# Kernel optimization log

Hardware: AMD Instinct MI355X
Metric: run time of the kernel (lower is better)

Reference implementation:

```python
import jax, jax.numpy as jnp
import numpy as np

N = 40000          # nodes
E = 640000         # edges (avg degree 16)
MUL = 32           # multiplicity per irrep
SILU_GAIN = 1.6791 # e3nn normalize2mom constant for silu
SQ3 = float(np.sqrt(3.0)); SQ2 = float(np.sqrt(2.0))
C_S = float(np.sin(np.pi / 8)); C_X = float(np.cos(np.pi / 8))
INV_SQRT_NN = 1.0 / 4.0  # 1/sqrt(num_neighbors=16)


def _fctp_scalar_attr(xs, xv, W0, W1, na):
    # FullyConnectedTensorProduct(irreps, '1x0e', irreps): per-l linear scaled by
    # the scalar attr, with e3nn fan-in normalization 1/sqrt(mul_in).
    f0 = 1.0 / np.sqrt(W0.shape[0]); f1 = 1.0 / np.sqrt(W1.shape[0])
    ss = (xs @ W0) * f0 * na                                   # [N, w]
    sv = jnp.einsum('nui,uw->nwi', xv, W1) * f1 * na[..., None]  # [N, w, 3]
    return ss, sv


def _forward(node_input, node_attr, edge_index, edge_attr, edge_scalars,
             W_sc0, W_sc1, W_l10, W_l11, Wfc0, Wfc1, W_l20, W_l21):
    na = node_attr[:, :1]                               # [N,1] scalar 0e attr
    xs = node_input[:, :MUL]                            # [N,32]  0e
    xv = node_input[:, MUL:].reshape(-1, MUL, 3)        # [N,32,3] 1o

    # self-connection and first linear (both FCTP with scalar node attr)
    s_s, s_v = _fctp_scalar_attr(xs, xv, W_sc0, W_sc1, na)
    l_s, l_v = _fctp_scalar_attr(xs, xv, W_l10, W_l11, na)

    # radial MLP -> per-edge TP weights (weight_numel = 5*32 = 160)
    h = jax.nn.silu(edge_scalars @ Wfc0 / 4.0) * SILU_GAIN   # /sqrt(16)
    w = (h @ Wfc1) / 8.0                                     # /sqrt(64), [E,160]
    w0, w1, w2, w3, w4 = [w[:, k * MUL:(k + 1) * MUL] for k in range(5)]

    src, dst = edge_index[0], edge_index[1]
    xs_e = l_s[src]                                     # gather [E,32]
    xv_e = l_v[src]                                     # gather [E,32,3]
    ea0 = edge_attr[:, 0:1]                             # [E,1]  0e
    eav = edge_attr[:, 1:4]                             # [E,3]  1o

    # 'uvu' CG tensor product paths (mid irreps sorted: 64x0e + 96x1o)
    mid0 = w0 * xs_e * ea0                                             # 0e x 0e -> 0e
    mid1 = w3 * jnp.einsum('eui,ei->eu', xv_e, eav) / SQ3              # 1o x 1o -> 0e
    mid2 = (w1 * xs_e)[..., None] * eav[:, None, :]                    # 0e x 1o -> 1o
    mid3 = w2[..., None] * xv_e * ea0[..., None]                       # 1o x 0e -> 1o
    mid4 = w4[..., None] * jnp.cross(xv_e, eav[:, None, :]) / SQ2      # 1o x 1o -> 1o

    mid_s = jnp.concatenate([mid0, mid1], axis=1)                      # [E,64]
    mid_v = jnp.concatenate([mid2, mid3, mid4], axis=1)                # [E,96,3]

    # scatter-reduce to destination nodes
    node_s = jax.ops.segment_sum(mid_s, dst, num_segments=N) * INV_SQRT_NN
    node_v = jax.ops.segment_sum(mid_v, dst, num_segments=N) * INV_SQRT_NN

    # lin2: FCTP(mid, 1x0e, out)
    x2_s = (node_s @ W_l20) / np.sqrt(64.0) * na
    x2_v = jnp.einsum('nui,uw->nwi', node_v, W_l21) / np.sqrt(96.0) * na[..., None]

    # sc output mask is all ones here -> c_x = cos(pi/8) everywhere
    out_s = C_S * s_s + C_X * x2_s
    out_v = C_S * s_v + C_X * x2_v
    return jnp.concatenate([out_s, out_v.reshape(-1, MUL * 3)], axis=1)  # [N,128]


def setup_inputs() -> dict:
    key = jax.random.key(0)
    ks = jax.random.split(key, 13)
    return {
        'node_input': jax.random.normal(ks[0], (N, 128), jnp.float32),
        'node_attr': jax.random.normal(ks[1], (N, 1), jnp.float32),
        'edge_index': jax.random.randint(ks[2], (2, E), 0, N),
        'edge_attr': jax.random.normal(ks[3], (E, 4), jnp.float32),
        'edge_scalars': jax.random.normal(ks[4], (E, 16), jnp.float32),
        'W_sc0': jax.random.normal(ks[5], (32, 32), jnp.float32),
        'W_sc1': jax.random.normal(ks[6], (32, 32), jnp.float32),
        'W_l10': jax.random.normal(ks[7], (32, 32), jnp.float32),
        'W_l11': jax.random.normal(ks[8], (32, 32), jnp.float32),
        'Wfc0': jax.random.normal(ks[9], (16, 64), jnp.float32),
        'Wfc1': jax.random.normal(ks[10], (64, 160), jnp.float32),
        'W_l20': jax.random.normal(ks[11], (64, 32), jnp.float32),
        'W_l21': jax.random.normal(ks[12], (96, 32), jnp.float32),
    }


def reference(node_input, node_attr, edge_index, edge_attr, edge_scalars,
              W_sc0, W_sc1, W_l10, W_l11, Wfc0, Wfc1, W_l20, W_l21):
    return _forward(node_input, node_attr, edge_index, edge_attr, edge_scalars,
                    W_sc0, W_sc1, W_l10, W_l11, Wfc0, Wfc1, W_l20, W_l21)
```

## Files before the change

### kernel.cpp

```cpp
#include <hip/hip_runtime.h>
#include <math.h>

static constexpr float F0        = 0.17677669529663687f;
static constexpr float SILU_GAIN = 1.6791f;
static constexpr float INV_SQ3   = 0.5773502691896258f;
static constexpr float INV_SQ2   = 0.7071067811865475f;
static constexpr float C_S       = 0.3826834323650898f;
static constexpr float C_X       = 0.9238795325112867f;
static constexpr float INV_SQRT_NN = 0.25f;
static constexpr float INV8      = 0.125f;
static constexpr float INV_SQ96  = 0.10206207261596575f;

#define WAVE_SYNC() do { asm volatile("" ::: "memory"); \
                         __builtin_amdgcn_wave_barrier(); \
                         asm volatile("" ::: "memory"); } while (0)

__global__ __launch_bounds__(256) void k_node(
    const float* __restrict__ node_input, const float* __restrict__ node_attr,
    const float* __restrict__ Wsc0, const float* __restrict__ Wsc1,
    const float* __restrict__ Wl10, const float* __restrict__ Wl11,
    float* __restrict__ out, float* __restrict__ l_sv, int N)
{
    __shared__ float sW[4][32][32];
    __shared__ __align__(16) float sX[4][128];
    int tid = threadIdx.x;
    float4* sWv = (float4*)&sW[0][0][0];
    for (int i = tid; i < 256; i += 256) {
        sWv[i]       = ((const float4*)Wsc0)[i];
        sWv[256+i]   = ((const float4*)Wsc1)[i];
        sWv[512+i]   = ((const float4*)Wl10)[i];
        sWv[768+i]   = ((const float4*)Wl11)[i];
    }
    __syncthreads();
    int wave = tid >> 6, lane = tid & 63;
    int ngroups = (N + 3) >> 2;

    for (int grp = blockIdx.x; grp < ngroups; grp += gridDim.x) {
        int node = grp * 4 + wave;
        if (node >= N) continue;

        float2 v = *(const float2*)&node_input[(size_t)node*128 + lane*2];
        sX[wave][lane*2]   = v.x;
        sX[wave][lane*2+1] = v.y;
        float na = node_attr[node];
        WAVE_SYNC();

        const float* X = sX[wave];
        float g = F0 * na;
        #pragma unroll
        for (int p = 0; p < 2; p++) {
            int o = lane + p*64;
            float vs = 0.f, vl = 0.f;
            if (o < 32) {
                #pragma unroll
                for (int u = 0; u < 32; u++) {
                    float x = X[u];
                    vs = fmaf(x, sW[0][u][o], vs);
                    vl = fmaf(x, sW[2][u][o], vl);
                }
            } else {
                int f = o - 32; int w = f / 3; int i3 = f - 3*w;
                #pragma unroll
                for (int u = 0; u < 32; u++) {
                    float x = X[32 + 3*u + i3];
                    vs = fmaf(x, sW[1][u][w], vs);
                    vl = fmaf(x, sW[3][u][w], vl);
                }
            }
            out [(size_t)node*128 + o] = C_S * g * vs;
            l_sv[(size_t)node*128 + o] = g * vl;
        }
        WAVE_SYNC();
    }
}

__global__ void k_hist(const int* __restrict__ ei, int* __restrict__ deg, int E) {
    int e = blockIdx.x*256 + threadIdx.x;
    if (e < E) atomicAdd(&deg[ei[E + e]], 1);
}

__global__ void k_scan_part(const int* __restrict__ deg, int* __restrict__ offs,
                            int* __restrict__ part, int n) {
    __shared__ int tmp[1024];
    int t = threadIdx.x, i = blockIdx.x*1024 + t;
    int v = (i < n) ? deg[i] : 0;
    tmp[t] = v; __syncthreads();
    for (int d = 1; d < 1024; d <<= 1) {
        int x = (t >= d) ? tmp[t-d] : 0;
        __syncthreads();
        tmp[t] += x;
        __syncthreads();
    }
    if (i < n) offs[i] = tmp[t] - v;
    if (t == 1023) part[blockIdx.x] = tmp[1023];
}

__global__ void k_scan_top(int* part, int* offs, int nb, int n) {
    if (threadIdx.x == 0 && blockIdx.x == 0) {
        int run = 0;
        for (int b = 0; b < nb; b++) { int v = part[b]; part[b] = run; run += v; }
        offs[n] = run;
    }
}

__global__ void k_scan_add(int* offs, const int* part, int n) {
    int i = blockIdx.x*256 + threadIdx.x;
    if (i < n) offs[i] += part[i >> 10];
}

__global__ void k_fill(const int* __restrict__ ei, const int* __restrict__ offs,
                       int* __restrict__ cur, int* __restrict__ elist, int E) {
    int e = blockIdx.x*256 + threadIdx.x;
    if (e < E) {
        int d = ei[E + e];
        int p = atomicAdd(&cur[d], 1);
        elist[offs[d] + p] = e;
    }
}

__global__ __launch_bounds__(256, 3) void k_edge(
    const int*   __restrict__ ei,
    const float* __restrict__ edge_attr,
    const float* __restrict__ edge_scalars,
    const float* __restrict__ Wfc0,
    const float* __restrict__ Wfc1,
    const float* __restrict__ W20,
    const float* __restrict__ W21,
    const float* __restrict__ node_attr,
    const float* __restrict__ l_sv,
    const int*   __restrict__ offs,
    const int*   __restrict__ elist,
    float* __restrict__ out, int N, int E)
{
    __shared__ float sWfc1[64][160];
    __shared__ __align__(16) float sH [4][8][64];
    __shared__ __align__(16) float sES[4][8][16];
    __shared__ float sEA[4][8][4];
    __shared__ int   sSRC[4][8];

    int tid = threadIdx.x;
    {
        float4* dst = (float4*)&sWfc1[0][0];
        const float4* src = (const float4*)Wfc1;
        for (int i = tid; i < 2560; i += 256) dst[i] = src[i];
    }

    int wave = tid >> 6, lane = tid & 63;
    int half = lane >> 5, u = lane & 31;

    float wfc0_r[16];
    #pragma unroll
    for (int i = 0; i < 16; i++) wfc0_r[i] = Wfc0[i*64 + lane];

    __syncthreads();

    int ngroups = (N + 3) >> 2;
    int es_e = lane >> 3, es_i2 = (lane & 7) << 1;

    for (int grp = blockIdx.x; grp < ngroups; grp += gridDim.x) {
        int node = grp * 4 + wave;
        if (node >= N) continue;

        int e0 = offs[node], e1 = offs[node+1];
        int cnt_all = e1 - e0;
        const int* mylist = elist + e0;
        float na = node_attr[node];

        float a0 = 0.f, a1 = 0.f;
        float av0[3] = {0,0,0}, av1[3] = {0,0,0}, av2[3] = {0,0,0};

        int    r_src;
        float4 r_ea;
        float2 r_es;
        #define STAGE_REGS(B) do {                                               \
            bool v8 = (lane < 8) && ((B) + lane < cnt_all);                      \
            int eidA = v8 ? mylist[(B) + lane] : 0;                              \
            r_src = v8 ? ei[eidA] : 0;                                           \
            r_ea  = v8 ? *(const float4*)&edge_attr[(size_t)eidA*4]              \
                       : make_float4(0.f,0.f,0.f,0.f);                           \
            bool ve = ((B) + es_e) < cnt_all;                                    \
            int eidB = ve ? mylist[(B) + es_e] : 0;                              \
            r_es = ve ? *(const float2*)&edge_scalars[(size_t)eidB*16 + es_i2]   \
                      : make_float2(0.f,0.f);                                    \
        } while (0)

        STAGE_REGS(0);

        for (int base = 0; base < cnt_all; base += 8) {
            if (lane < 8) {
                sSRC[wave][lane] = r_src;
                sEA[wave][lane][0] = r_ea.x; sEA[wave][lane][1] = r_ea.y;
                sEA[wave][lane][2] = r_ea.z; sEA[wave][lane][3] = r_ea.w;
            }
            sES[wave][es_e][es_i2]   = r_es.x;
            sES[wave][es_e][es_i2+1] = r_es.y;
            WAVE_SYNC();

            STAGE_REGS(base + 8);

            float xs_r[4], xv_r[4][3];
            #pragma unroll
            for (int t = 0; t < 4; t++) {
                int srcn = sSRC[wave][half*4 + t];
                const float* lp = l_sv + (size_t)srcn * 128;
                xs_r[t]    = lp[u];
                xv_r[t][0] = lp[32 + 3*u];
                xv_r[t][1] = lp[33 + 3*u];
                xv_r[t][2] = lp[34 + 3*u];
            }

            #pragma unroll
            for (int e = 0; e < 8; e++) {
                float s = 0.f;
                const float4* esv = (const float4*)sES[wave][e];
                #pragma unroll
                for (int i4 = 0; i4 < 4; i4++) {
                    float4 ev = esv[i4];
                    s = fmaf(ev.x, wfc0_r[i4*4+0], s);
                    s = fmaf(ev.y, wfc0_r[i4*4+1], s);
                    s = fmaf(ev.z, wfc0_r[i4*4+2], s);
                    s = fmaf(ev.w, wfc0_r[i4*4+3], s);
                }
                s *= 0.25f;
                sH[wave][e][lane] = SILU_GAIN * s / (1.f + __expf(-s));
            }
            WAVE_SYNC();

            float w0[4] = {0,0,0,0}, w1[4] = {0,0,0,0}, w2[4] = {0,0,0,0};
            float w3[4] = {0,0,0,0}, w4[4] = {0,0,0,0};
            #pragma unroll 2
            for (int j = 0; j < 64; j += 4) {
                float4 hv0 = *(const float4*)&sH[wave][half*4+0][j];
                float4 hv1 = *(const float4*)&sH[wave][half*4+1][j];
                float4 hv2 = *(const float4*)&sH[wave][half*4+2][j];
                float4 hv3 = *(const float4*)&sH[wave][half*4+3][j];
                float h0[4] = {hv0.x, hv0.y, hv0.z, hv0.w};
                float h1[4] = {hv1.x, hv1.y, hv1.z, hv1.w};
                float h2[4] = {hv2.x, hv2.y, hv2.z, hv2.w};
                float h3[4] = {hv3.x, hv3.y, hv3.z, hv3.w};
                #pragma unroll
                for (int jj = 0; jj < 4; jj++) {
                    float c0 = sWfc1[j+jj][u];
                    float c1 = sWfc1[j+jj][32+u];
                    float c2 = sWfc1[j+jj][64+u];
                    float c3 = sWfc1[j+jj][96+u];
                    float c4 = sWfc1[j+jj][128+u];
                    w0[0]=fmaf(h0[jj],c0,w0[0]); w1[0]=fmaf(h0[jj],c1,w1[0]); w2[0]=fmaf(h0[jj],c2,w2[0]); w3[0]=fmaf(h0[jj],c3,w3[0]); w4[0]=fmaf(h0[jj],c4,w4[0]);
                    w0[1]=fmaf(h1[jj],c0,w0[1]); w1[1]=fmaf(h1[jj],c1,w1[1]); w2[1]=fmaf(h1[jj],c2,w2[1]); w3[1]=fmaf(h1[jj],c3,w3[1]); w4[1]=fmaf(h1[jj],c4,w4[1]);
                    w0[2]=fmaf(h2[jj],c0,w0[2]); w1[2]=fmaf(h2[jj],c1,w1[2]); w2[2]=fmaf(h2[jj],c2,w2[2]); w3[2]=fmaf(h2[jj],c3,w3[2]); w4[2]=fmaf(h2[jj],c4,w4[2]);
                    w0[3]=fmaf(h3[jj],c0,w0[3]); w1[3]=fmaf(h3[jj],c1,w1[3]); w2[3]=fmaf(h3[jj],c2,w2[3]); w3[3]=fmaf(h3[jj],c3,w3[3]); w4[3]=fmaf(h3[jj],c4,w4[3]);
                }
            }

            #pragma unroll
            for (int t = 0; t < 4; t++) {
                int ee = half*4 + t;
                float ea0 = sEA[wave][ee][0];
                float ev0 = sEA[wave][ee][1], ev1 = sEA[wave][ee][2], ev2 = sEA[wave][ee][3];
                float xs  = xs_r[t];
                float xv0 = xv_r[t][0], xv1 = xv_r[t][1], xv2 = xv_r[t][2];
                float W0 = w0[t]*INV8, W1 = w1[t]*INV8, W2 = w2[t]*INV8;
                float W3 = w3[t]*INV8, W4 = w4[t]*INV8;

                a0 = fmaf(W0 * ea0, xs, a0);
                float dv = fmaf(xv0, ev0, fmaf(xv1, ev1, xv2*ev2));
                a1 = fmaf(W3 * INV_SQ3, dv, a1);
                float t1 = W1 * xs;
                av0[0] = fmaf(t1, ev0, av0[0]); av0[1] = fmaf(t1, ev1, av0[1]); av0[2] = fmaf(t1, ev2, av0[2]);
                float t2 = W2 * ea0;
                av1[0] = fmaf(t2, xv0, av1[0]); av1[1] = fmaf(t2, xv1, av1[1]); av1[2] = fmaf(t2, xv2, av1[2]);
                float cr0 = xv1*ev2 - xv2*ev1;
                float cr1 = xv2*ev0 - xv0*ev2;
                float cr2 = xv0*ev1 - xv1*ev0;
                float t4 = W4 * INV_SQ2;
                av2[0] = fmaf(t4, cr0, av2[0]); av2[1] = fmaf(t4, cr1, av2[1]); av2[2] = fmaf(t4, cr2, av2[2]);
            }
            WAVE_SYNC();
        }
        #undef STAGE_REGS

        a0 += __shfl_xor(a0, 32, 64);
        a1 += __shfl_xor(a1, 32, 64);
        #pragma unroll
        for (int i = 0; i < 3; i++) {
            av0[i] += __shfl_xor(av0[i], 32, 64);
            av1[i] += __shfl_xor(av1[i], 32, 64);
            av2[i] += __shfl_xor(av2[i], 32, 64);
        }
        float* sc = &sH[wave][0][0];
        if (half == 0) {
            sc[u] = a0; sc[32+u] = a1;
            #pragma unroll
            for (int i = 0; i < 3; i++) {
                sc[64 + 3*u + i]        = av0[i];
                sc[64 + 96 + 3*u + i]   = av1[i];
                sc[64 + 192 + 3*u + i]  = av2[i];
            }
        }
        WAVE_SYNC();

        float gs = C_X * na * INV_SQRT_NN * INV8;
        float gv = C_X * na * INV_SQRT_NN * INV_SQ96;
        #pragma unroll
        for (int p = 0; p < 2; p++) {
            int o = lane + p*64;
            float val = 0.f;
            if (o < 32) {
                #pragma unroll 8
                for (int k = 0; k < 64; k++) val = fmaf(sc[k], W20[k*32 + o], val);
                out[(size_t)node*128 + o] += gs * val;
            } else {
                int f = o - 32; int w = f / 3; int i3 = f - 3*w;
                #pragma unroll 8
                for (int k = 0; k < 96; k++) val = fmaf(sc[64 + 3*k + i3], W21[k*32 + w], val);
                out[(size_t)node*128 + o] += gv * val;
            }
        }
        WAVE_SYNC();
    }
}

extern "C" void kernel_launch(void* const* d_in, const int* in_sizes, int n_in,
                              void* d_out, int out_size, void* d_ws, size_t ws_size,
                              hipStream_t stream)
{
    const float* node_input   = (const float*)d_in[0];
    const float* node_attr    = (const float*)d_in[1];
    const int*   edge_index   = (const int*)  d_in[2];
    const float* edge_attr    = (const float*)d_in[3];
    const float* edge_scalars = (const float*)d_in[4];
    const float* W_sc0 = (const float*)d_in[5];
    const float* W_sc1 = (const float*)d_in[6];
    const float* W_l10 = (const float*)d_in[7];
    const float* W_l11 = (const float*)d_in[8];
    const float* Wfc0  = (const float*)d_in[9];
    const float* Wfc1  = (const float*)d_in[10];
    const float* W_l20 = (const float*)d_in[11];
    const float* W_l21 = (const float*)d_in[12];
    float* out = (float*)d_out;

    int N = in_sizes[1];
    int E = in_sizes[2] / 2;

    char* ws = (char*)d_ws;
    size_t off = 0;
    float* l_sv  = (float*)(ws + off); off += (size_t)N * 128 * 4;
    int*   deg   = (int*)  (ws + off); off += (size_t)N * 4;
    int*   cur   = (int*)  (ws + off); off += (size_t)N * 4;
    int*   offs  = (int*)  (ws + off); off += ((size_t)N + 1) * 4;
    off = (off + 255) & ~(size_t)255;
    int*   elist = (int*)  (ws + off); off += (size_t)E * 4;
    int*   part  = (int*)  (ws + off); off += 64 * 4;

    hipMemsetAsync(deg, 0, (size_t)N * 2 * 4, stream);

    int ngroups = (N + 3) / 4;
    int nb_node = ngroups < 1024 ? ngroups : 1024;
    k_node<<<nb_node, 256, 0, stream>>>(node_input, node_attr, W_sc0, W_sc1, W_l10, W_l11,
                                        out, l_sv, N);
    k_hist<<<(E + 255)/256, 256, 0, stream>>>(edge_index, deg, E);
    int nchunk = (N + 1023) / 1024;
    k_scan_part<<<nchunk, 1024, 0, stream>>>(deg, offs, part, N);
    k_scan_top<<<1, 64, 0, stream>>>(part, offs, nchunk, N);
    k_scan_add<<<(N + 255)/256, 256, 0, stream>>>(offs, part, N);
    k_fill<<<(E + 255)/256, 256, 0, stream>>>(edge_index, offs, cur, elist, E);
    int nb_edge = ngroups < 1536 ? ngroups : 1536;
    k_edge<<<nb_edge, 256, 0, stream>>>(edge_index, edge_attr, edge_scalars,
                                        Wfc0, Wfc1, W_l20, W_l21,
                                        node_attr, l_sv, offs, elist, out, N, E);
}
```

Measured before the change: 692.0 us.

## Drop scan-add kernel, transpose and swizzle Wfc1 in LDS, vectorize loads

```diff
diff --git a/kernel.cpp b/kernel.cpp
--- a/kernel.cpp
+++ b/kernel.cpp
@@ -95,26 +95,21 @@
     if (t == 1023) part[blockIdx.x] = tmp[1023];
 }
 
-__global__ void k_scan_top(int* part, int* offs, int nb, int n) {
+__global__ void k_scan_top(int* part, int nb) {
     if (threadIdx.x == 0 && blockIdx.x == 0) {
         int run = 0;
         for (int b = 0; b < nb; b++) { int v = part[b]; part[b] = run; run += v; }
-        offs[n] = run;
-    }
-}
-
-__global__ void k_scan_add(int* offs, const int* part, int n) {
-    int i = blockIdx.x*256 + threadIdx.x;
-    if (i < n) offs[i] += part[i >> 10];
+    }
 }
 
 __global__ void k_fill(const int* __restrict__ ei, const int* __restrict__ offs,
+                       const int* __restrict__ part,
                        int* __restrict__ cur, int* __restrict__ elist, int E) {
     int e = blockIdx.x*256 + threadIdx.x;
     if (e < E) {
         int d = ei[E + e];
         int p = atomicAdd(&cur[d], 1);
-        elist[offs[d] + p] = e;
+        elist[offs[d] + part[d >> 10] + p] = e;
     }
 }
 
@@ -129,20 +124,20 @@
     const float* __restrict__ node_attr,
     const float* __restrict__ l_sv,
     const int*   __restrict__ offs,
+    const int*   __restrict__ part,
     const int*   __restrict__ elist,
     float* __restrict__ out, int N, int E)
 {
-    __shared__ float sWfc1[64][160];
+    __shared__ float sWfc1T[160][64];
     __shared__ __align__(16) float sH [4][8][64];
     __shared__ __align__(16) float sES[4][8][16];
     __shared__ float sEA[4][8][4];
     __shared__ int   sSRC[4][8];
 
     int tid = threadIdx.x;
-    {
-        float4* dst = (float4*)&sWfc1[0][0];
-        const float4* src = (const float4*)Wfc1;
-        for (int i = tid; i < 2560; i += 256) dst[i] = src[i];
+    for (int idx = tid; idx < 10240; idx += 256) {
+        int j = idx / 160, c = idx - 160*j;
+        sWfc1T[c][2*(((j>>1)) ^ (c & 31)) + (j & 1)] = Wfc1[idx];
     }
 
     int wave = tid >> 6, lane = tid & 63;
@@ -161,7 +156,8 @@
         int node = grp * 4 + wave;
         if (node >= N) continue;
 
-        int e0 = offs[node], e1 = offs[node+1];
+        int e0 = offs[node] + part[node >> 10];
+        int e1 = (node + 1 < N) ? (offs[node+1] + part[(node+1) >> 10]) : E;
         int cnt_all = e1 - e0;
         const int* mylist = elist + e0;
         float na = node_attr[node];
@@ -203,10 +199,9 @@
             for (int t = 0; t < 4; t++) {
                 int srcn = sSRC[wave][half*4 + t];
                 const float* lp = l_sv + (size_t)srcn * 128;
-                xs_r[t]    = lp[u];
-                xv_r[t][0] = lp[32 + 3*u];
-                xv_r[t][1] = lp[33 + 3*u];
-                xv_r[t][2] = lp[34 + 3*u];
+                xs_r[t] = lp[u];
+                float3 v3 = *(const float3*)&lp[32 + 3*u];
+                xv_r[t][0] = v3.x; xv_r[t][1] = v3.y; xv_r[t][2] = v3.z;
             }
 
             #pragma unroll
@@ -222,14 +217,15 @@
                     s = fmaf(ev.w, wfc0_r[i4*4+3], s);
                 }
                 s *= 0.25f;
-                sH[wave][e][lane] = SILU_GAIN * s / (1.f + __expf(-s));
+                sH[wave][e][lane] = SILU_GAIN * s * __builtin_amdgcn_rcpf(1.f + __expf(-s));
             }
             WAVE_SYNC();
 
             float w0[4] = {0,0,0,0}, w1[4] = {0,0,0,0}, w2[4] = {0,0,0,0};
             float w3[4] = {0,0,0,0}, w4[4] = {0,0,0,0};
             #pragma unroll 2
-            for (int j = 0; j < 64; j += 4) {
+            for (int jb4 = 0; jb4 < 16; jb4++) {
+                int j = jb4 * 4;
                 float4 hv0 = *(const float4*)&sH[wave][half*4+0][j];
                 float4 hv1 = *(const float4*)&sH[wave][half*4+1][j];
                 float4 hv2 = *(const float4*)&sH[wave][half*4+2][j];
@@ -238,13 +234,18 @@
                 float h1[4] = {hv1.x, hv1.y, hv1.z, hv1.w};
                 float h2[4] = {hv2.x, hv2.y, hv2.z, hv2.w};
                 float h3[4] = {hv3.x, hv3.y, hv3.z, hv3.w};
+                float c[5][4];
+                int b0 = (2*jb4) ^ u, b1 = (2*jb4 + 1) ^ u;
+                #pragma unroll
+                for (int q = 0; q < 5; q++) {
+                    const float* Tc = &sWfc1T[q*32 + u][0];
+                    float2 f2a = *(const float2*)&Tc[2*b0];
+                    float2 f2b = *(const float2*)&Tc[2*b1];
+                    c[q][0] = f2a.x; c[q][1] = f2a.y; c[q][2] = f2b.x; c[q][3] = f2b.y;
+                }
                 #pragma unroll
                 for (int jj = 0; jj < 4; jj++) {
-                    float c0 = sWfc1[j+jj][u];
-                    float c1 = sWfc1[j+jj][32+u];
-                    float c2 = sWfc1[j+jj][64+u];
-                    float c3 = sWfc1[j+jj][96+u];
-                    float c4 = sWfc1[j+jj][128+u];
+                    float c0 = c[0][jj], c1 = c[1][jj], c2 = c[2][jj], c3 = c[3][jj], c4 = c[4][jj];
                     w0[0]=fmaf(h0[jj],c0,w0[0]); w1[0]=fmaf(h0[jj],c1,w1[0]); w2[0]=fmaf(h0[jj],c2,w2[0]); w3[0]=fmaf(h0[jj],c3,w3[0]); w4[0]=fmaf(h0[jj],c4,w4[0]);
                     w0[1]=fmaf(h1[jj],c0,w0[1]); w1[1]=fmaf(h1[jj],c1,w1[1]); w2[1]=fmaf(h1[jj],c2,w2[1]); w3[1]=fmaf(h1[jj],c3,w3[1]); w4[1]=fmaf(h1[jj],c4,w4[1]);
                     w0[2]=fmaf(h2[jj],c0,w0[2]); w1[2]=fmaf(h2[jj],c1,w1[2]); w2[2]=fmaf(h2[jj],c2,w2[2]); w3[2]=fmaf(h2[jj],c3,w3[2]); w4[2]=fmaf(h2[jj],c4,w4[2]);
@@ -361,11 +362,10 @@
     k_hist<<<(E + 255)/256, 256, 0, stream>>>(edge_index, deg, E);
     int nchunk = (N + 1023) / 1024;
     k_scan_part<<<nchunk, 1024, 0, stream>>>(deg, offs, part, N);
-    k_scan_top<<<1, 64, 0, stream>>>(part, offs, nchunk, N);
-    k_scan_add<<<(N + 255)/256, 256, 0, stream>>>(offs, part, N);
-    k_fill<<<(E + 255)/256, 256, 0, stream>>>(edge_index, offs, cur, elist, E);
+    k_scan_top<<<1, 64, 0, stream>>>(part, nchunk);
+    k_fill<<<(E + 255)/256, 256, 0, stream>>>(edge_index, offs, part, cur, elist, E);
     int nb_edge = ngroups < 1536 ? ngroups : 1536;
     k_edge<<<nb_edge, 256, 0, stream>>>(edge_index, edge_attr, edge_scalars,
                                         Wfc0, Wfc1, W_l20, W_l21,
-                                        node_attr, l_sv, offs, elist, out, N, E);
-}
+                                        node_attr, l_sv, offs, part, elist, out, N, E);
+}
```

Result: faster. 669.0 us (-3.3%).
